# Kernel optimization log

Measured on AMD Instinct MI355X. Metric: run time of the kernel, lower is better.

The kernel has to match this reference:

```python
import jax, jax.numpy as jnp
import numpy as np

D = 1024      # d_model
H = 16        # num_heads
HW = D // H   # head_width = 64
FF = 4 * D    # hidden_dim = 4096
BATCH = 2
T = 2048
EPS = 1e-5


def layer_norm(x, g, b):
    mu = jnp.mean(x, axis=-1, keepdims=True)
    var = jnp.mean(jnp.square(x - mu), axis=-1, keepdims=True)
    return (x - mu) * jax.lax.rsqrt(var + EPS) * g + b


def setup_inputs() -> dict:
    key = jax.random.key(0)
    ks = jax.random.split(key, 7)
    s = 0.02
    return {
        "x": jax.random.normal(ks[0], (BATCH, T, D), dtype=jnp.float32),
        "Wq": jax.random.normal(ks[1], (D, D), dtype=jnp.float32) * s,
        "Wk": jax.random.normal(ks[2], (D, D), dtype=jnp.float32) * s,
        "Wv": jax.random.normal(ks[3], (D, D), dtype=jnp.float32) * s,
        "W1": jax.random.normal(ks[4], (FF, D), dtype=jnp.float32) * s,
        "W2": jax.random.normal(ks[5], (D, FF), dtype=jnp.float32) * s,
        "g1": jnp.ones((D,), dtype=jnp.float32),
        "b1": jnp.zeros((D,), dtype=jnp.float32),
        "g2": jnp.ones((D,), dtype=jnp.float32),
        "b2": jnp.zeros((D,), dtype=jnp.float32),
    }


def reference(x, Wq, Wk, Wv, W1, W2, g1, b1, g2, b2):
    N, t, d = x.shape
    # norm1
    xn = layer_norm(x, g1, b1)

    # --- MHSA with ALiBi + causal mask (math mirrors torch module) ---
    def heads(y):  # (N,t,D) -> (N,H,t,HW)
        return y.reshape(N, t, H, HW).transpose(0, 2, 1, 3)

    q = heads(xn @ Wq.T)
    k = heads(xn @ Wk.T)
    v = heads(xn @ Wv.T)

    scores = jnp.einsum("nhqd,nhkd->nhqk", q, k) / np.sqrt(HW).astype(np.float32)

    pos = jnp.arange(t)
    rel = (pos[None, :] - pos[:, None]).astype(x.dtype)           # [t,t], rel[i,j]=j-i
    slopes = (2.0 ** (-(jnp.arange(1, H + 1)) * (8.0 / H))).astype(x.dtype)  # [H]
    alibi = slopes[:, None, None] * rel                            # [H,t,t]
    causal = jnp.where(pos[None, :] > pos[:, None],
                       jnp.array(-jnp.inf, x.dtype),
                       jnp.array(0.0, x.dtype))                    # [t,t]

    att = jax.nn.softmax(scores + alibi[None] + causal[None, None], axis=-1)
    o = jnp.einsum("nhqk,nhkd->nhqd", att, v)
    o = o.transpose(0, 2, 1, 3).reshape(N, t, d)

    att_out = xn + o

    # --- MLP: Linear -> SiLU -> Linear ---
    h = layer_norm(att_out, g2, b2)
    m = jax.nn.silu(h @ W1.T) @ W2.T
    return att_out + m
```

## Files before the change

kernel.cpp:

```cpp
#include <hip/hip_runtime.h>

#define DMODEL 1024
#define NHEAD  16
#define HWID   64
#define FFDIM  4096
#define NBATCH 2
#define SEQT   2048
#define NTOK   4096
#define QKLD   3072

using bf8    = __attribute__((ext_vector_type(8))) short;
using f32x4  = __attribute__((ext_vector_type(4))) float;
using f32x16 = __attribute__((ext_vector_type(16))) float;

__device__ inline short to_bf16(float f) {
  unsigned u = __float_as_uint(f);
  return (short)((u + 0x7fffu + ((u >> 16) & 1u)) >> 16);
}
__device__ inline float from_bf16(short s) {
  return __uint_as_float(((unsigned)(unsigned short)s) << 16);
}
__device__ inline float exp2_fast(float x) {
  float r;
  asm("v_exp_f32 %0, %1" : "=v"(r) : "v"(x));
  return r;
}
__device__ inline unsigned cvt_pk_bf16(float lo, float hi) {
  unsigned r;
  asm("v_cvt_pk_bf16_f32 %0, %1, %2" : "=v"(r) : "v"(lo), "v"(hi));
  return r;
}
__device__ inline void lds_load16(const void* g, void* l) {
  __builtin_amdgcn_global_load_lds(
      (const __attribute__((address_space(1))) void*)g,
      (__attribute__((address_space(3))) void*)l, 16, 0, 0);
}

__global__ __launch_bounds__(256)
void prep_kernel(const float* __restrict__ Wq, const float* __restrict__ Wk,
                 const float* __restrict__ Wv, const float* __restrict__ W1,
                 const float* __restrict__ W2, short* __restrict__ wqkv,
                 short* __restrict__ w1b, short* __restrict__ w2b,
                 const float* __restrict__ x, const float* __restrict__ g1,
                 const float* __restrict__ b1, short* __restrict__ xn) {
  __shared__ float red[8];
  if (blockIdx.x < 11264) {
    int i = blockIdx.x * 256 + threadIdx.x;
    const float* src;
    short* dst;
    if (i < 1048576)      { src = W1; dst = w1b; }
    else if (i < 2097152) { src = W2; dst = w2b;            i -= 1048576; }
    else if (i < 2359296) { src = Wq; dst = wqkv;           i -= 2097152; }
    else if (i < 2621440) { src = Wk; dst = wqkv + 1048576; i -= 2359296; }
    else                  { src = Wv; dst = wqkv + 2097152; i -= 2621440; }
    float4 v = ((const float4*)src)[i];
    short4 o;
    o.x = to_bf16(v.x); o.y = to_bf16(v.y);
    o.z = to_bf16(v.z); o.w = to_bf16(v.w);
    ((short4*)dst)[i] = o;
  } else {
    const int row = blockIdx.x - 11264;
    const int t = threadIdx.x;
    const float4 v = ((const float4*)(x + (long)row * DMODEL))[t];
    float s  = v.x + v.y + v.z + v.w;
    float s2 = v.x * v.x + v.y * v.y + v.z * v.z + v.w * v.w;
#pragma unroll
    for (int m = 1; m < 64; m <<= 1) {
      s  += __shfl_xor(s, m);
      s2 += __shfl_xor(s2, m);
    }
    if ((t & 63) == 0) { red[t >> 6] = s; red[4 + (t >> 6)] = s2; }
    __syncthreads();
    s  = red[0] + red[1] + red[2] + red[3];
    s2 = red[4] + red[5] + red[6] + red[7];
    const float mu = s * (1.f / DMODEL);
    const float rs = rsqrtf(s2 * (1.f / DMODEL) - mu * mu + 1e-5f);
    const float4 gv = ((const float4*)g1)[t];
    const float4 bv = ((const float4*)b1)[t];
    short4 o;
    o.x = to_bf16((v.x - mu) * rs * gv.x + bv.x);
    o.y = to_bf16((v.y - mu) * rs * gv.y + bv.y);
    o.z = to_bf16((v.z - mu) * rs * gv.z + bv.z);
    o.w = to_bf16((v.w - mu) * rs * gv.w + bv.w);
    ((short4*)(xn + (long)row * DMODEL))[t] = o;
  }
}

__global__ __launch_bounds__(256)
void ln_kernel(const float* __restrict__ x, const float* __restrict__ g,
               const float* __restrict__ b, short* __restrict__ out) {
  const int row = blockIdx.x;
  const int t = threadIdx.x;
  const float4 v = ((const float4*)(x + (long)row * DMODEL))[t];
  float s  = v.x + v.y + v.z + v.w;
  float s2 = v.x * v.x + v.y * v.y + v.z * v.z + v.w * v.w;
#pragma unroll
  for (int m = 1; m < 64; m <<= 1) {
    s  += __shfl_xor(s, m);
    s2 += __shfl_xor(s2, m);
  }
  __shared__ float red[8];
  if ((t & 63) == 0) { red[t >> 6] = s; red[4 + (t >> 6)] = s2; }
  __syncthreads();
  s  = red[0] + red[1] + red[2] + red[3];
  s2 = red[4] + red[5] + red[6] + red[7];
  const float mu = s * (1.f / DMODEL);
  const float rs = rsqrtf(s2 * (1.f / DMODEL) - mu * mu + 1e-5f);
  const float4 gv = ((const float4*)g)[t];
  const float4 bv = ((const float4*)b)[t];
  short4 o;
  o.x = to_bf16((v.x - mu) * rs * gv.x + bv.x);
  o.y = to_bf16((v.y - mu) * rs * gv.y + bv.y);
  o.z = to_bf16((v.z - mu) * rs * gv.z + bv.z);
  o.w = to_bf16((v.w - mu) * rs * gv.w + bv.w);
  ((short4*)(out + (long)row * DMODEL))[t] = o;
}

template <int EPI>
__global__ __launch_bounds__(512, 2)
void gemm256(const short* __restrict__ A, const short* __restrict__ Bw,
             void* __restrict__ Cout, int N, int lda, int ldb, int Kslice,
             long zstride) {
  __shared__ short lds[2][2][16384];
  const int tid = threadIdx.x;
  const int wid = tid >> 6, lane = tid & 63;
  const int l15 = lane & 15, l4 = lane >> 4;
  const int wm = wid >> 2, wn = wid & 3;

  const int gx = gridDim.x, nwg = gx * gridDim.y;
  const int wg = blockIdx.y * gx + blockIdx.x;
  const int sw = (wg & 7) * (nwg >> 3) + (wg >> 3);
  const int sx = gx >> 2;
  const int st = sw >> 4, w16 = sw & 15;
  const long bm = (long)((st / sx) * 4 + (w16 >> 2)) * 256;
  const long bn = (long)((st % sx) * 4 + (w16 & 3)) * 256;
  const long kofs = (long)blockIdx.z * Kslice;
  const int NT = Kslice >> 6;

  long arow[2], brow[2];
  int  sgel[2], dofs[2];
#pragma unroll
  for (int l = 0; l < 2; ++l) {
    const int g = l * 512 + tid;
    const int row = g >> 2;
    sgel[l] = ((g & 3) ^ ((row >> 1) & 3)) * 8;
    dofs[l] = g * 16;
    arow[l] = (bm + row) * (long)lda + kofs;
    brow[l] = (bn + row) * (long)ldb + kofs;
  }
  auto stage_half = [&](int h) {
    if (h >= (NT << 2)) return;
    const int th = h >> 2, hi = h & 3, buf = th & 1;
    const int ks = hi >> 1, isA = hi & 1;
    char* db = (char*)&lds[buf][isA ? 0 : 1][0] + ks * 16384;
    const long kb = (long)th * 64 + ks * 32;
#pragma unroll
    for (int l = 0; l < 2; ++l) {
      const short* src = (isA ? A + arow[l] : Bw + brow[l]) + kb + sgel[l];
      lds_load16(src, db + dofs[l]);
    }
  };

  const int xsw = (l4 ^ ((l15 >> 1) & 3)) << 4;
  const int aofs = (wm * 128 + l15) * 64 + xsw;
  const int bofs = (wn * 64 + l15) * 64 + xsw;

  f32x4 acc[8][4] = {};
  bf8 fa[4], fa2[4], fb[4];

#define PH_MID                                             \
  __builtin_amdgcn_s_barrier();                            \
  __builtin_amdgcn_s_setprio(1);
#define PH_END                                             \
  __builtin_amdgcn_s_setprio(0);                           \
  __builtin_amdgcn_s_barrier();                            \
  asm volatile("" ::: "memory");

#pragma unroll
  for (int h = 0; h < 7; ++h) stage_half(h);
  asm volatile("s_waitcnt vmcnt(6)" ::: "memory");
  __builtin_amdgcn_s_barrier();
  asm volatile("" ::: "memory");

  for (int u = 0; u < NT; ++u) {
    const int buf = u & 1;
    const char* pa = (const char*)&lds[buf][0][0];
    const char* pb = (const char*)&lds[buf][1][0];
#pragma unroll
    for (int m = 0; m < 4; ++m) fa[m] = *(const bf8*)(pa + aofs + m * 1024);
#pragma unroll
    for (int n = 0; n < 4; ++n) fb[n] = *(const bf8*)(pb + bofs + n * 1024);
    stage_half(4 * u + 7);
    PH_MID
#pragma unroll
    for (int m = 0; m < 4; ++m)
#pragma unroll
      for (int n = 0; n < 4; ++n)
        acc[m][n] = __builtin_amdgcn_mfma_f32_16x16x32_bf16(fa[m], fb[n], acc[m][n], 0, 0, 0);
    PH_END
#pragma unroll
    for (int m = 0; m < 4; ++m) fa2[m] = *(const bf8*)(pa + aofs + (4 + m) * 1024);
    stage_half(4 * u + 8);
    PH_MID
#pragma unroll
    for (int m = 0; m < 4; ++m)
#pragma unroll
      for (int n = 0; n < 4; ++n)
        acc[4 + m][n] = __builtin_amdgcn_mfma_f32_16x16x32_bf16(fa2[m], fb[n], acc[4 + m][n], 0, 0, 0);
    PH_END
#pragma unroll
    for (int m = 0; m < 4; ++m) fa[m] = *(const bf8*)(pa + 16384 + aofs + m * 1024);
#pragma unroll
    for (int n = 0; n < 4; ++n) fb[n] = *(const bf8*)(pb + 16384 + bofs + n * 1024);
    stage_half(4 * u + 9);
    PH_MID
#pragma unroll
    for (int m = 0; m < 4; ++m)
#pragma unroll
      for (int n = 0; n < 4; ++n)
        acc[m][n] = __builtin_amdgcn_mfma_f32_16x16x32_bf16(fa[m], fb[n], acc[m][n], 0, 0, 0);
    PH_END
#pragma unroll
    for (int m = 0; m < 4; ++m) fa2[m] = *(const bf8*)(pa + 16384 + aofs + (4 + m) * 1024);
    stage_half(4 * u + 10);
    if (u <= NT - 3)      asm volatile("s_waitcnt vmcnt(6)" ::: "memory");
    else if (u == NT - 2) asm volatile("s_waitcnt vmcnt(0)" ::: "memory");
    PH_MID
#pragma unroll
    for (int m = 0; m < 4; ++m)
#pragma unroll
      for (int n = 0; n < 4; ++n)
        acc[4 + m][n] = __builtin_amdgcn_mfma_f32_16x16x32_bf16(fa2[m], fb[n], acc[4 + m][n], 0, 0, 0);
    PH_END
  }
#undef PH_MID
#undef PH_END

#pragma unroll
  for (int mg = 0; mg < 8; ++mg)
#pragma unroll
    for (int n = 0; n < 4; ++n) {
      const long col = bn + wn * 64 + n * 16 + l15;
#pragma unroll
      for (int r = 0; r < 4; ++r) {
        const long row = bm + wm * 128 + mg * 16 + l4 * 4 + r;
        float v = acc[mg][n][r];
        if (EPI == 0) {
          ((short*)Cout)[row * N + col] = to_bf16(v);
        } else if (EPI == 1) {
          ((short*)Cout)[row * N + col] = to_bf16(v / (1.f + __expf(-v)));
        } else {
          ((short*)Cout)[blockIdx.z * zstride + row * N + col] = to_bf16(v);
        }
      }
    }
}

__global__ __launch_bounds__(256)
void pack_kv(const short* __restrict__ qkv, short* __restrict__ Kp,
             short* __restrict__ Vp) {
  __shared__ short tile[64][72];
  const int bx = blockIdx.x, bh = blockIdx.y;
  const int b = bh >> 4, h = bh & 15;
  const int t = threadIdx.x;
  if (bx < 64) {
    const int g = bx;
    const int row = t >> 3, cc = t & 7, c = cc >> 1, hi = cc & 1;
    const bf8 v = *(const bf8*)&qkv[(long)(b * SEQT + g * 32 + row) * QKLD +
                                    1024 + h * HWID + c * 16 + hi * 8];
    *(bf8*)&Kp[(((long)bh * 256 + g * 4 + c) * 64 + hi * 32 + row) * 8] = v;
  } else {
    const int tc = bx - 64;
    {
      const int r = t >> 2, c = (t & 3) * 16;
      const long src = (long)(b * SEQT + tc * 64 + r) * QKLD + 2048 + h * HWID + c;
      *(bf8*)&tile[r][c]     = *(const bf8*)&qkv[src];
      *(bf8*)&tile[r][c + 8] = *(const bf8*)&qkv[src + 8];
    }
    __syncthreads();
    const int dg = t >> 7, ch = (t >> 5) & 3, row = t & 31;
#pragma unroll
    for (int hi = 0; hi < 2; ++hi) {
      short o[8];
#pragma unroll
      for (int j = 0; j < 8; ++j) o[j] = tile[ch * 16 + hi * 8 + j][dg * 32 + row];
      *(bf8*)&Vp[(((long)bh * 256 + dg * 128 + tc * 4 + ch) * 64 + hi * 32 + row) * 8] =
          *(bf8*)o;
    }
  }
}

__global__ __launch_bounds__(64, 2)
void attn_kernel(const short* __restrict__ qkv, const short* __restrict__ Kp,
                 const short* __restrict__ Vp, const short* __restrict__ xn,
                 float* __restrict__ att) {
  const int L = blockIdx.x;
  const int bh = (L & 7) * 4 + ((L >> 3) & 3);
  const int u = L >> 5;
  const int qtile = (u < 32) ? (63 - u) : (u - 32);
  const int b = bh >> 4, h = bh & 15;
  const int q0 = qtile * 32;
  const int lane = threadIdx.x;
  const int l31 = lane & 31, hi = lane >> 5;
  const long tokbase = (long)b * SEQT;

  bf8 qf[4];
  {
    const short* qrow = qkv + (tokbase + q0 + l31) * QKLD + h * HWID + hi * 8;
#pragma unroll
    for (int c = 0; c < 4; ++c) qf[c] = *(const bf8*)(qrow + c * 16);
  }

  const float slope2 = exp2f(-0.5f * (float)(h + 1)) * 1.44269504f;
  const float sc2 = 0.125f * 1.44269504f;
  float arr[16];
#pragma unroll
  for (int r = 0; r < 16; ++r) arr[r] = slope2 * (float)((r & 3) + 8 * (r >> 2));
  const float hofs = slope2 * 4.f * (float)hi;
  const float qabs = (float)(q0 + l31);

  float m2 = -1e30f, lsum = 0.f;
  f32x16 acc0 = {}, acc1 = {};
  const int ktm = q0 >> 6;
  const bf8* kfb = (const bf8*)Kp + (long)bh * 16384 + lane;
  const bf8* vfb = (const bf8*)Vp + (long)bh * 16384 + lane;

  bf8 kc[8], kn[8], vc[8];
#pragma unroll
  for (int c = 0; c < 4; ++c) {
    kc[c]     = kfb[c * 64];
    kc[4 + c] = kfb[256 + c * 64];
  }

#pragma unroll 2
  for (int kt = 0; kt <= ktm; ++kt) {
    const int k0 = kt * 64;
    const long vb = (long)kt * 256;
#pragma unroll
    for (int ch = 0; ch < 4; ++ch) {
      vc[ch]     = vfb[vb + ch * 64];
      vc[4 + ch] = vfb[8192 + vb + ch * 64];
    }
    const long nb = (long)(kt < ktm ? kt + 1 : kt) * 512;
#pragma unroll
    for (int c = 0; c < 4; ++c) {
      kn[c]     = kfb[nb + c * 64];
      kn[4 + c] = kfb[nb + 256 + c * 64];
    }
    f32x16 s0 = {}, s1 = {};
#pragma unroll
    for (int c = 0; c < 4; ++c) {
      s0 = __builtin_amdgcn_mfma_f32_32x32x16_bf16(kc[c], qf[c], s0, 0, 0, 0);
      s1 = __builtin_amdgcn_mfma_f32_32x32x16_bf16(kc[4 + c], qf[c], s1, 0, 0, 0);
    }
    const float base = slope2 * ((float)k0 - qabs) + hofs;
    float s[32];
#pragma unroll
    for (int r = 0; r < 16; ++r) {
      s[r]      = fmaf(s0[r], sc2, base + arr[r]);
      s[16 + r] = fmaf(s1[r], sc2, base + arr[r] + slope2 * 32.f);
    }
    if (kt == ktm) {
      const int qi = q0 + l31;
#pragma unroll
      for (int r = 0; r < 16; ++r) {
        const int krel = (r & 3) + 8 * (r >> 2) + 4 * hi;
        if (k0 + krel > qi)      s[r]      = -1e30f;
        if (k0 + 32 + krel > qi) s[16 + r] = -1e30f;
      }
    }
    float ma = s[0], mb = s[1], mc = s[2], md = s[3];
#pragma unroll
    for (int i = 4; i < 32; i += 4) {
      ma = fmaxf(ma, s[i]); mb = fmaxf(mb, s[i + 1]);
      mc = fmaxf(mc, s[i + 2]); md = fmaxf(md, s[i + 3]);
    }
    float pm = fmaxf(fmaxf(ma, mb), fmaxf(mc, md));
    pm = fmaxf(pm, __shfl_xor(pm, 32));
    if (!__all(pm - m2 <= 11.0f)) {
      const float nm = fmaxf(m2, pm);
      const float alpha = exp2_fast(m2 - nm);
      m2 = nm;
      lsum *= alpha;
      acc0 *= alpha;
      acc1 *= alpha;
    }
    float p[32];
#pragma unroll
    for (int i = 0; i < 32; ++i) p[i] = exp2_fast(s[i] - m2);
    float sa = p[0], sb = p[1], sc = p[2], sd = p[3];
#pragma unroll
    for (int i = 4; i < 32; i += 4) {
      sa += p[i]; sb += p[i + 1]; sc += p[i + 2]; sd += p[i + 3];
    }
    float rs = (sa + sb) + (sc + sd);
    rs += __shfl_xor(rs, 32);
    lsum += rs;
    unsigned cpk[16];
#pragma unroll
    for (int g = 0; g < 8; ++g) {
      cpk[g]     = cvt_pk_bf16(p[2 * g], p[2 * g + 1]);
      cpk[8 + g] = cvt_pk_bf16(p[16 + 2 * g], p[16 + 2 * g + 1]);
    }
    bf8 pb[4];
#pragma unroll
    for (int ch = 0; ch < 4; ++ch) {
      const int cb = (ch >> 1) * 8 + (ch & 1) * 4;
      unsigned u0 = cpk[cb + 0], u2 = cpk[cb + 2];
      unsigned u1 = cpk[cb + 1], u3 = cpk[cb + 3];
      asm("v_permlane32_swap_b32 %0, %1" : "+v"(u0), "+v"(u2));
      asm("v_permlane32_swap_b32 %0, %1" : "+v"(u1), "+v"(u3));
      union { unsigned u[4]; bf8 v; } f;
      f.u[0] = u0; f.u[1] = u1; f.u[2] = u2; f.u[3] = u3;
      pb[ch] = f.v;
    }
#pragma unroll
    for (int ch = 0; ch < 4; ++ch) {
      acc0 = __builtin_amdgcn_mfma_f32_32x32x16_bf16(vc[ch], pb[ch], acc0, 0, 0, 0);
      acc1 = __builtin_amdgcn_mfma_f32_32x32x16_bf16(vc[4 + ch], pb[ch], acc1, 0, 0, 0);
    }
#pragma unroll
    for (int i = 0; i < 8; ++i) kc[i] = kn[i];
  }

  __shared__ float Os[32 * 68];
  const float rl = 1.f / lsum;
#pragma unroll
  for (int r = 0; r < 16; ++r) {
    const int d0 = (r & 3) + 8 * (r >> 2) + 4 * hi;
    Os[l31 * 68 + d0]      = acc0[r] * rl;
    Os[l31 * 68 + 32 + d0] = acc1[r] * rl;
  }
  __syncthreads();
#pragma unroll
  for (int it = 0; it < 8; ++it) {
    const int idx = it * 64 + lane;
    const int row = idx >> 4, c4 = idx & 15;
    const float4 ov = *(const float4*)&Os[row * 68 + c4 * 4];
    const long gbase = (tokbase + q0 + row) * DMODEL + h * HWID + c4 * 4;
    const short4 xv = *(const short4*)&xn[gbase];
    float4 o;
    o.x = ov.x + from_bf16(xv.x);
    o.y = ov.y + from_bf16(xv.y);
    o.z = ov.z + from_bf16(xv.z);
    o.w = ov.w + from_bf16(xv.w);
    *(float4*)&att[gbase] = o;
  }
}

__global__ __launch_bounds__(256)
void combine_kernel(const short* __restrict__ p, float* __restrict__ dout, int n4) {
  int i = blockIdx.x * 256 + threadIdx.x;
  if (i < n4) {
    float4 a = ((const float4*)dout)[i];
    short4 b0 = ((const short4*)(p))[i];
    short4 b1 = ((const short4*)(p + 4194304))[i];
    short4 b2 = ((const short4*)(p + 8388608))[i];
    short4 b3 = ((const short4*)(p + 12582912))[i];
    a.x += (from_bf16(b0.x) + from_bf16(b1.x)) + (from_bf16(b2.x) + from_bf16(b3.x));
    a.y += (from_bf16(b0.y) + from_bf16(b1.y)) + (from_bf16(b2.y) + from_bf16(b3.y));
    a.z += (from_bf16(b0.z) + from_bf16(b1.z)) + (from_bf16(b2.z) + from_bf16(b3.z));
    a.w += (from_bf16(b0.w) + from_bf16(b1.w)) + (from_bf16(b2.w) + from_bf16(b3.w));
    ((float4*)dout)[i] = a;
  }
}

extern "C" void kernel_launch(void* const* d_in, const int* in_sizes, int n_in,
                              void* d_out, int out_size, void* d_ws, size_t ws_size,
                              hipStream_t stream) {
  (void)in_sizes; (void)n_in; (void)out_size; (void)ws_size;
  const float* x  = (const float*)d_in[0];
  const float* Wq = (const float*)d_in[1];
  const float* Wk = (const float*)d_in[2];
  const float* Wv = (const float*)d_in[3];
  const float* W1 = (const float*)d_in[4];
  const float* W2 = (const float*)d_in[5];
  const float* g1 = (const float*)d_in[6];
  const float* b1 = (const float*)d_in[7];
  const float* g2 = (const float*)d_in[8];
  const float* b2 = (const float*)d_in[9];

  char* ws = (char*)d_ws;
  const size_t MB = 1024 * 1024;
  short* wqkv_b = (short*)(ws + 0);
  short* w1_b   = (short*)(ws + 6  * MB);
  short* w2_b   = (short*)(ws + 14 * MB);
  short* xn     = (short*)(ws + 22 * MB);
  short* qkv    = (short*)(ws + 30 * MB);
  short* m1     = (short*)(ws + 22 * MB);
  short* Kp     = (short*)(ws + 54 * MB);
  short* Vp     = (short*)(ws + 62 * MB);
  short* hb     = (short*)(ws + 70 * MB);
  short* parts  = (short*)(ws + 54 * MB);
  float* att    = (float*)d_out;

  prep_kernel<<<15360, 256, 0, stream>>>(Wq, Wk, Wv, W1, W2, wqkv_b, w1_b, w2_b,
                                         x, g1, b1, xn);

  gemm256<0><<<dim3(12, 16), 512, 0, stream>>>(xn, wqkv_b, qkv, QKLD, DMODEL, DMODEL,
                                               DMODEL, 0);
  pack_kv<<<dim3(96, 32), 256, 0, stream>>>(qkv, Kp, Vp);

  attn_kernel<<<2048, 64, 0, stream>>>(qkv, Kp, Vp, xn, att);

  ln_kernel<<<NTOK, 256, 0, stream>>>(att, g2, b2, hb);

  gemm256<1><<<dim3(16, 16), 512, 0, stream>>>(hb, w1_b, m1, FFDIM, DMODEL, DMODEL,
                                               DMODEL, 0);
  gemm256<2><<<dim3(4, 16, 4), 512, 0, stream>>>(m1, w2_b, parts, DMODEL, FFDIM, FFDIM,
                                                 1024, (long)NTOK * DMODEL);
  combine_kernel<<<4096, 256, 0, stream>>>(parts, (float*)d_out, 1048576);
}
```

Before: 197.0 us.

## Pack four causal q-tiles per 256-thread attention block for load balance

The attention kernel now launches 512 blocks of 4 wavefronts instead of 2048 single-wave blocks. Each wave takes a q-tile chosen so that short and long causal tiles (i, 63-i, 31-i, 32+i) share a block, which balances work per block and cuts block count and scheduling overhead. The shared output staging buffer becomes per-wave, and the __syncthreads is dropped since each wave only reads its own slice. The risk is that the higher occupancy requirement under launch bounds (256,2) raises register pressure, and that the removed barrier relies on intra-wave LDS ordering.

```diff
diff --git a/kernel.cpp b/kernel.cpp
--- a/kernel.cpp
+++ b/kernel.cpp
@@ -290,17 +290,19 @@
   }
 }
 
-__global__ __launch_bounds__(64, 2)
+__global__ __launch_bounds__(256, 2)
 void attn_kernel(const short* __restrict__ qkv, const short* __restrict__ Kp,
                  const short* __restrict__ Vp, const short* __restrict__ xn,
                  float* __restrict__ att) {
+  __shared__ float Os[4][32 * 68];
   const int L = blockIdx.x;
   const int bh = (L & 7) * 4 + ((L >> 3) & 3);
-  const int u = L >> 5;
-  const int qtile = (u < 32) ? (63 - u) : (u - 32);
+  const int i = L >> 5;
+  const int w = threadIdx.x >> 6;
+  const int qtile = (w == 0) ? i : (w == 1) ? 63 - i : (w == 2) ? 31 - i : 32 + i;
   const int b = bh >> 4, h = bh & 15;
   const int q0 = qtile * 32;
-  const int lane = threadIdx.x;
+  const int lane = threadIdx.x & 63;
   const int l31 = lane & 31, hi = lane >> 5;
   const long tokbase = (long)b * SEQT;
 
@@ -371,9 +373,9 @@
     }
     float ma = s[0], mb = s[1], mc = s[2], md = s[3];
 #pragma unroll
-    for (int i = 4; i < 32; i += 4) {
-      ma = fmaxf(ma, s[i]); mb = fmaxf(mb, s[i + 1]);
-      mc = fmaxf(mc, s[i + 2]); md = fmaxf(md, s[i + 3]);
+    for (int i2 = 4; i2 < 32; i2 += 4) {
+      ma = fmaxf(ma, s[i2]); mb = fmaxf(mb, s[i2 + 1]);
+      mc = fmaxf(mc, s[i2 + 2]); md = fmaxf(md, s[i2 + 3]);
     }
     float pm = fmaxf(fmaxf(ma, mb), fmaxf(mc, md));
     pm = fmaxf(pm, __shfl_xor(pm, 32));
@@ -387,11 +389,11 @@
     }
     float p[32];
 #pragma unroll
-    for (int i = 0; i < 32; ++i) p[i] = exp2_fast(s[i] - m2);
+    for (int i2 = 0; i2 < 32; ++i2) p[i2] = exp2_fast(s[i2] - m2);
     float sa = p[0], sb = p[1], sc = p[2], sd = p[3];
 #pragma unroll
-    for (int i = 4; i < 32; i += 4) {
-      sa += p[i]; sb += p[i + 1]; sc += p[i + 2]; sd += p[i + 3];
+    for (int i2 = 4; i2 < 32; i2 += 4) {
+      sa += p[i2]; sb += p[i2 + 1]; sc += p[i2 + 2]; sd += p[i2 + 3];
     }
     float rs = (sa + sb) + (sc + sd);
     rs += __shfl_xor(rs, 32);
@@ -420,23 +422,22 @@
       acc1 = __builtin_amdgcn_mfma_f32_32x32x16_bf16(vc[4 + ch], pb[ch], acc1, 0, 0, 0);
     }
 #pragma unroll
-    for (int i = 0; i < 8; ++i) kc[i] = kn[i];
-  }
-
-  __shared__ float Os[32 * 68];
+    for (int i2 = 0; i2 < 8; ++i2) kc[i2] = kn[i2];
+  }
+
+  float* os = &Os[w][0];
   const float rl = 1.f / lsum;
 #pragma unroll
   for (int r = 0; r < 16; ++r) {
     const int d0 = (r & 3) + 8 * (r >> 2) + 4 * hi;
-    Os[l31 * 68 + d0]      = acc0[r] * rl;
-    Os[l31 * 68 + 32 + d0] = acc1[r] * rl;
-  }
-  __syncthreads();
+    os[l31 * 68 + d0]      = acc0[r] * rl;
+    os[l31 * 68 + 32 + d0] = acc1[r] * rl;
+  }
 #pragma unroll
   for (int it = 0; it < 8; ++it) {
     const int idx = it * 64 + lane;
     const int row = idx >> 4, c4 = idx & 15;
-    const float4 ov = *(const float4*)&Os[row * 68 + c4 * 4];
+    const float4 ov = *(const float4*)&os[row * 68 + c4 * 4];
     const long gbase = (tokbase + q0 + row) * DMODEL + h * HWID + c4 * 4;
     const short4 xv = *(const short4*)&xn[gbase];
     float4 o;
@@ -501,7 +502,7 @@
                                                DMODEL, 0);
   pack_kv<<<dim3(96, 32), 256, 0, stream>>>(qkv, Kp, Vp);
 
-  attn_kernel<<<2048, 64, 0, stream>>>(qkv, Kp, Vp, xn, att);
+  attn_kernel<<<512, 256, 0, stream>>>(qkv, Kp, Vp, xn, att);
 
   ln_kernel<<<NTOK, 256, 0, stream>>>(att, g2, b2, hb);
 
```

Measured after the change: 198.9 us. Within noise of the previous version (+0.9%).
